# Kernel optimization log

Hardware: AMD Instinct MI355X
Metric: run time of the kernel (lower is better)

The kernel has to match this reference:

```python
import jax, jax.numpy as jnp
import numpy as np

N_FFT = 1024
HOP = 256
WIN = 1024
SIG_LEN = 16777216  # 2**24 samples


def _hamming_sym(M):
    # scipy.signal.hamming(M, sym=True): 0.54 - 0.46*cos(2*pi*n/(M-1))
    n = np.arange(M)
    return (0.54 - 0.46 * np.cos(2.0 * np.pi * n / (M - 1))).astype(np.float32)


def setup_inputs() -> dict:
    key = jax.random.key(0)
    x = jax.random.normal(key, (SIG_LEN,), dtype=jnp.float32)
    return {"x": x}


def reference(x):
    # window, normalized by sqrt(n_fft) (sum of Hamming window is nonzero)
    win = jnp.asarray(_hamming_sym(WIN) / np.sqrt(N_FFT).astype(np.float32))
    hw2 = WIN // 2
    half_n = N_FFT // 2 + 1
    pad = 3 * HOP

    xp = jnp.pad(x, (pad, pad))       # np.append zeros on both sides
    total = xp.shape[0]
    n_rows = total // HOP             # allocated output rows (trailing rows stay zero)
    n_frames = (total - WIN) // HOP + 1  # frames actually computed by the while-loop

    starts = jnp.arange(n_frames) * HOP
    frames = xp[starts[:, None] + jnp.arange(WIN)[None, :]] * win

    # zero-phase buffer: buf[:hw1] = win_x[hw2:], buf[-hw2:] = win_x[:hw2]
    mid = jnp.zeros((n_frames, N_FFT - WIN), dtype=frames.dtype)
    buf = jnp.concatenate([frames[:, hw2:], mid, frames[:, :hw2]], axis=1)

    spec = jnp.fft.rfft(buf, n=N_FFT, axis=1)        # [n_frames, half_n] complex64
    mag = jnp.abs(spec).astype(jnp.float32)
    ph = jnp.angle(spec).astype(jnp.float32)

    xm_x = jnp.zeros((n_rows, half_n), jnp.float32).at[:n_frames].set(mag)
    xp_x = jnp.zeros((n_rows, half_n), jnp.float32).at[:n_frames].set(ph)
    return (xm_x, xp_x)
```

## Files before the change

kernel.cpp:

```cpp
#include <hip/hip_runtime.h>


#define SIG_LEN   16777216
#define N_FRAMES  65539
#define N_ROWS    65542
#define HALF_N    513
#define FRAMES_FLOATS (N_FRAMES * HALF_N)
#define MAG_SZ        (N_ROWS   * HALF_N)


__global__ void init_tables(double* __restrict__ ws) {
  int i = blockIdx.x * 256 + threadIdx.x;
  const double PI = 3.14159265358979323846;
  if (i < 1024) {
    ws[i] = (0.54 - 0.46 * cos(2.0 * PI * (double)i / 1023.0)) / 32.0;
  }
  if (i < 448) {
    int l = i / 7, r = i % 7 + 1;
    double a = -2.0 * PI * (double)(l * r) / 512.0;
    ws[1024 + 2 * i]     = cos(a);
    ws[1024 + 2 * i + 1] = sin(a);
  }
  if (i < 56) {
    int q = i / 7, r = i % 7 + 1;
    double a = -2.0 * PI * (double)(8 * q * r) / 512.0;
    ws[1920 + 2 * i]     = cos(a);
    ws[1920 + 2 * i + 1] = sin(a);
  }
  if (i < 513) {
    double th = PI * (double)i / 512.0;
    double c = cos(th), s = sin(th);
    ws[2048 + 4 * i]     = 0.5 * (1.0 - s);
    ws[2048 + 4 * i + 1] = -0.5 * c;
    ws[2048 + 4 * i + 2] = 0.5 * (1.0 + s);
    ws[2048 + 4 * i + 3] = 0.5 * c;
  }
}

__global__ void zero_tail(float* __restrict__ out) {
  int i = blockIdx.x * 256 + threadIdx.x;
  if (i < (MAG_SZ - FRAMES_FLOATS)) {
    out[FRAMES_FLOATS + i] = 0.0f;
    out[MAG_SZ + FRAMES_FLOATS + i] = 0.0f;
  }
}

#define CMUL(vr, vi, wx, wy) { double _t = (vr)*(wx) - (vi)*(wy); \
                               (vi) = (vr)*(wy) + (vi)*(wx); (vr) = _t; }

__device__ __forceinline__ void dft8(double* ar, double* ai) {
  const double S = 0.70710678118654752440;
  double s0r = ar[0] + ar[4], s0i = ai[0] + ai[4];
  double s1r = ar[0] - ar[4], s1i = ai[0] - ai[4];
  double s2r = ar[2] + ar[6], s2i = ai[2] + ai[6];
  double s3r = ar[2] - ar[6], s3i = ai[2] - ai[6];
  double t0r = ar[1] + ar[5], t0i = ai[1] + ai[5];
  double t1r = ar[1] - ar[5], t1i = ai[1] - ai[5];
  double t2r = ar[3] + ar[7], t2i = ai[3] + ai[7];
  double t3r = ar[3] - ar[7], t3i = ai[3] - ai[7];

  double e0r = s0r + s2r, e0i = s0i + s2i;
  double e2r = s0r - s2r, e2i = s0i - s2i;
  double e1r = s1r + s3i, e1i = s1i - s3r;
  double e3r = s1r - s3i, e3i = s1i + s3r;
  double o0r = t0r + t2r, o0i = t0i + t2i;
  double o2r = t0r - t2r, o2i = t0i - t2i;
  double o1r = t1r + t3i, o1i = t1i - t3r;
  double o3r = t1r - t3i, o3i = t1i + t3r;

  double u1r = S * (o1r + o1i), u1i = S * (o1i - o1r);
  double u2r = o2i,             u2i = -o2r;
  double u3r = S * (o3i - o3r), u3i = -S * (o3r + o3i);

  ar[0] = e0r + o0r; ai[0] = e0i + o0i;
  ar[4] = e0r - o0r; ai[4] = e0i - o0i;
  ar[1] = e1r + u1r; ai[1] = e1i + u1i;
  ar[5] = e1r - u1r; ai[5] = e1i - u1i;
  ar[2] = e2r + u2r; ai[2] = e2i + u2i;
  ar[6] = e2r - u2r; ai[6] = e2i - u2i;
  ar[3] = e3r + u3r; ai[3] = e3i + u3i;
  ar[7] = e3r - u3r; ai[7] = e3i - u3i;
}

__device__ __forceinline__ float fast_atan2f(float y, float x) {
  const float PI   = 3.14159265358979f;
  const float PI_2 = 1.57079632679490f;
  float ax = fabsf(x), ay = fabsf(y);
  float mx = fmaxf(ax, ay), mn = fminf(ax, ay);
  float t = mn * __builtin_amdgcn_rcpf(mx);
  t = (mx == 0.0f) ? 0.0f : t;
  float zz = t * t;
  float a = fmaf(zz, -0.01172120f, 0.05265332f);
  a = fmaf(zz, a, -0.11643287f);
  a = fmaf(zz, a,  0.19354346f);
  a = fmaf(zz, a, -0.33262347f);
  a = fmaf(zz, a,  0.99997726f);
  a = a * t;
  a = (ay > ax) ? (PI_2 - a) : a;
  a = (x < 0.0f) ? (PI - a) : a;
  return copysignf(a, y);
}

__global__ __launch_bounds__(128, 5) void stft_frame(const float* __restrict__ x,
                                                     const double* __restrict__ ws,
                                                     float* __restrict__ out) {
  __shared__ double2 zbuf[2][512];

  const int wv = threadIdx.x >> 6;
  const int l  = threadIdx.x & 63;
  const int f  = blockIdx.x * 2 + wv;
  if (f >= N_FRAMES) return;
  double2* z = zbuf[wv];

  const int g = l >> 3;
  const int q = l & 7;

  double ar[8], ai[8];
  const int base = f * 256 - 768;
  if (base >= 0 && base + 1024 <= SIG_LEN) {
#pragma unroll
    for (int n2 = 0; n2 < 8; ++n2) {
      int j = 128 * n2 + 2 * l;
      float2 xv = *(const float2*)(x + base + j);
      double2 wn = *(const double2*)(ws + j);
      ar[n2] = (double)xv.x * wn.x;
      ai[n2] = (double)xv.y * wn.y;
    }
  } else {
#pragma unroll
    for (int n2 = 0; n2 < 8; ++n2) {
      int j  = 128 * n2 + 2 * l;
      int ix = base + j;
      double v0 = (ix >= 0 && ix < SIG_LEN) ? (double)x[ix] : 0.0;
      double v1 = (ix + 1 >= 0 && ix + 1 < SIG_LEN) ? (double)x[ix + 1] : 0.0;
      double2 wn = *(const double2*)(ws + j);
      ar[n2] = v0 * wn.x;
      ai[n2] = v1 * wn.y;
    }
  }

  dft8(ar, ai);
  {
    const double2* tw1 = (const double2*)(ws + 1024) + l * 7;
#pragma unroll
    for (int r = 1; r < 8; ++r) {
      double2 w = tw1[r - 1];
      CMUL(ar[r], ai[r], w.x, w.y);
    }
  }

#pragma unroll
  for (int r = 0; r < 8; ++r) {
    z[64 * r + 8 * g + (q ^ g)] = make_double2(ar[r], ai[r]);
  }
  asm volatile("s_waitcnt lgkmcnt(0)" ::: "memory");
#pragma unroll
  for (int r = 0; r < 8; ++r) {
    double2 v = z[64 * g + 8 * r + (q ^ r)];
    ar[r] = v.x; ai[r] = v.y;
  }

  dft8(ar, ai);
  {
    const double2* tw2 = (const double2*)(ws + 1920) + q * 7;
#pragma unroll
    for (int r = 1; r < 8; ++r) {
      double2 w = tw2[r - 1];
      CMUL(ar[r], ai[r], w.x, w.y);
    }
  }

#pragma unroll
  for (int r = 0; r < 8; ++r) {
    z[64 * g + 8 * r + (q ^ r)] = make_double2(ar[r], ai[r]);
  }
  asm volatile("s_waitcnt lgkmcnt(0)" ::: "memory");
#pragma unroll
  for (int r = 0; r < 8; ++r) {
    double2 v = z[64 * g + 8 * q + (r ^ q)];
    ar[r] = v.x; ai[r] = v.y;
  }

  dft8(ar, ai);

#pragma unroll
  for (int r = 0; r < 8; ++r) {
    z[64 * r + 8 * q + (g ^ q)] = make_double2(ar[r], ai[r]);
  }
  asm volatile("s_waitcnt lgkmcnt(0)" ::: "memory");

  const double* AB = ws + 2048;
  const int czk = 8 * g + (q ^ g);
  const float sgn = (l & 1) ? -1.0f : 1.0f;
  float* outm = out + f * HALF_N;
  float* outp = out + MAG_SZ + f * HALF_N;
#pragma unroll
  for (int i = 0; i < 4; ++i) {
    int k  = 64 * i + l;
    int km = 512 - k;
    double2 Zk = z[64 * i + czk];
    int zmi = km & 511;
    zmi = (zmi & ~7) | ((zmi ^ (zmi >> 3)) & 7);
    double2 Zm = z[zmi];
    const double* ab = AB + 4 * k;
    double Axv = ab[0], Ayv = ab[1], Bxv = ab[2], Byv = ab[3];
    double Yr  = Zk.x * Axv - Zk.y * Ayv + Zm.x * Bxv + Zm.y * Byv;
    double Yi  = Zk.x * Ayv + Zk.y * Axv + Zm.x * Byv - Zm.y * Bxv;
    double Y2r = Zm.x * Axv + Zm.y * Ayv + Zk.x * Bxv - Zk.y * Byv;
    double Y2i = -(Zm.x * Ayv - Zm.y * Axv + Zk.x * Byv + Zk.y * Bxv);
    if (i == 0) {
      if (l == 0) { Yi = 0.0; Y2i = 0.0; }
    }
    float yr  = (float)Yr,  yi  = (float)Yi;
    float y2r = (float)Y2r, y2i = (float)Y2i;
    float mag1 = __builtin_amdgcn_sqrtf(fmaf(yr, yr, yi * yi));
    float ph1  = fast_atan2f(sgn * yi, sgn * yr);
    float mag2 = __builtin_amdgcn_sqrtf(fmaf(y2r, y2r, y2i * y2i));
    float ph2  = fast_atan2f(sgn * y2i, sgn * y2r);
    outm[k]  = mag1;
    outp[k]  = ph1;
    outm[km] = mag2;
    outp[km] = ph2;
  }

  if (l == 0) {
    double2 zc = z[256];
    float yr = (float)zc.x, yi = (float)(-zc.y);
    outm[256] = __builtin_amdgcn_sqrtf(fmaf(yr, yr, yi * yi));
    outp[256] = fast_atan2f(yi, yr);
  }
}

extern "C" void kernel_launch(void* const* d_in, const int* in_sizes, int n_in,
                              void* d_out, int out_size, void* d_ws, size_t ws_size,
                              hipStream_t stream) {
  const float* x = (const float*)d_in[0];
  float* out = (float*)d_out;
  double* ws = (double*)d_ws;

  hipLaunchKernelGGL(init_tables, dim3(4), dim3(256), 0, stream, ws);
  hipLaunchKernelGGL(zero_tail, dim3(7), dim3(256), 0, stream, out);
  hipLaunchKernelGGL(stft_frame, dim3((N_FRAMES + 1) / 2), dim3(128), 0, stream,
                     x, ws, out);
}
```

Measured before the change: 400.1 us.

## Process two adjacent frames per wavefront, sharing input loads and twiddles

Each 64-thread block now computes two consecutive frames in one wavefront. It loads 10 float2 vectors covering both overlapping windows, so the shared samples are fetched once, and window/twiddle/AB coefficients are applied to both frames. The final-stage output mapping is changed so each lane keeps its own Zk in registers and only the mirrored Zm is read from LDS, with the odd-k sign folded into the AB table. This doubles register pressure per thread (launch bounds 64,4), which may reduce occupancy.

```diff
diff --git a/kernel.cpp b/kernel.cpp
--- a/kernel.cpp
+++ b/kernel.cpp
@@ -30,10 +30,11 @@
   if (i < 513) {
     double th = PI * (double)i / 512.0;
     double c = cos(th), s = sin(th);
-    ws[2048 + 4 * i]     = 0.5 * (1.0 - s);
-    ws[2048 + 4 * i + 1] = -0.5 * c;
-    ws[2048 + 4 * i + 2] = 0.5 * (1.0 + s);
-    ws[2048 + 4 * i + 3] = 0.5 * c;
+    double sg = (i & 1) ? -1.0 : 1.0;
+    ws[2048 + 4 * i]     = sg * 0.5 * (1.0 - s);
+    ws[2048 + 4 * i + 1] = sg * -0.5 * c;
+    ws[2048 + 4 * i + 2] = sg * 0.5 * (1.0 + s);
+    ws[2048 + 4 * i + 3] = sg * 0.5 * c;
   }
 }
 
@@ -101,133 +102,167 @@
   return copysignf(a, y);
 }
 
-__global__ __launch_bounds__(128, 5) void stft_frame(const float* __restrict__ x,
-                                                     const double* __restrict__ ws,
-                                                     float* __restrict__ out) {
-  __shared__ double2 zbuf[2][512];
-
-  const int wv = threadIdx.x >> 6;
-  const int l  = threadIdx.x & 63;
-  const int f  = blockIdx.x * 2 + wv;
-  if (f >= N_FRAMES) return;
-  double2* z = zbuf[wv];
-
+__global__ __launch_bounds__(64, 4) void stft_frame(const float* __restrict__ x,
+                                                    const double* __restrict__ ws,
+                                                    float* __restrict__ out) {
+  __shared__ double2 zA[512];
+  __shared__ double2 zB[512];
+
+  const int l = threadIdx.x;
   const int g = l >> 3;
   const int q = l & 7;
 
-  double ar[8], ai[8];
-  const int base = f * 256 - 768;
-  if (base >= 0 && base + 1024 <= SIG_LEN) {
-#pragma unroll
-    for (int n2 = 0; n2 < 8; ++n2) {
-      int j = 128 * n2 + 2 * l;
-      float2 xv = *(const float2*)(x + base + j);
-      double2 wn = *(const double2*)(ws + j);
-      ar[n2] = (double)xv.x * wn.x;
-      ai[n2] = (double)xv.y * wn.y;
-    }
+  const int fa = blockIdx.x * 2;
+  const int fb = fa + 1;
+  const bool bvalid = (fb < N_FRAMES);
+
+  float2 xv[10];
+  const int baseA = fa * 256 - 768;
+  if (baseA >= 0 && baseA + 1280 <= SIG_LEN) {
+#pragma unroll
+    for (int m = 0; m < 10; ++m)
+      xv[m] = *(const float2*)(x + baseA + 128 * m + 2 * l);
   } else {
 #pragma unroll
-    for (int n2 = 0; n2 < 8; ++n2) {
-      int j  = 128 * n2 + 2 * l;
-      int ix = base + j;
-      double v0 = (ix >= 0 && ix < SIG_LEN) ? (double)x[ix] : 0.0;
-      double v1 = (ix + 1 >= 0 && ix + 1 < SIG_LEN) ? (double)x[ix + 1] : 0.0;
-      double2 wn = *(const double2*)(ws + j);
-      ar[n2] = v0 * wn.x;
-      ai[n2] = v1 * wn.y;
-    }
-  }
-
-  dft8(ar, ai);
+    for (int m = 0; m < 10; ++m) {
+      int ix = baseA + 128 * m + 2 * l;
+      float a0 = (ix >= 0 && ix < SIG_LEN) ? x[ix] : 0.0f;
+      float a1 = (ix + 1 >= 0 && ix + 1 < SIG_LEN) ? x[ix + 1] : 0.0f;
+      xv[m] = make_float2(a0, a1);
+    }
+  }
+
+  double aar[8], aai[8], bar[8], bai[8];
+#pragma unroll
+  for (int n2 = 0; n2 < 8; ++n2) {
+    double2 wn = *(const double2*)(ws + 128 * n2 + 2 * l);
+    aar[n2] = (double)xv[n2].x     * wn.x;
+    aai[n2] = (double)xv[n2].y     * wn.y;
+    bar[n2] = (double)xv[n2 + 2].x * wn.x;
+    bai[n2] = (double)xv[n2 + 2].y * wn.y;
+  }
+
+  dft8(aar, aai);
+  dft8(bar, bai);
   {
     const double2* tw1 = (const double2*)(ws + 1024) + l * 7;
 #pragma unroll
     for (int r = 1; r < 8; ++r) {
       double2 w = tw1[r - 1];
-      CMUL(ar[r], ai[r], w.x, w.y);
-    }
-  }
-
-#pragma unroll
-  for (int r = 0; r < 8; ++r) {
-    z[64 * r + 8 * g + (q ^ g)] = make_double2(ar[r], ai[r]);
+      CMUL(aar[r], aai[r], w.x, w.y);
+      CMUL(bar[r], bai[r], w.x, w.y);
+    }
+  }
+
+#pragma unroll
+  for (int r = 0; r < 8; ++r) {
+    int e = 64 * r + 8 * g + (q ^ g);
+    zA[e] = make_double2(aar[r], aai[r]);
+    zB[e] = make_double2(bar[r], bai[r]);
   }
   asm volatile("s_waitcnt lgkmcnt(0)" ::: "memory");
 #pragma unroll
   for (int r = 0; r < 8; ++r) {
-    double2 v = z[64 * g + 8 * r + (q ^ r)];
-    ar[r] = v.x; ai[r] = v.y;
-  }
-
-  dft8(ar, ai);
+    int e = 64 * g + 8 * r + (q ^ r);
+    double2 va = zA[e], vb = zB[e];
+    aar[r] = va.x; aai[r] = va.y;
+    bar[r] = vb.x; bai[r] = vb.y;
+  }
+
+  dft8(aar, aai);
+  dft8(bar, bai);
   {
     const double2* tw2 = (const double2*)(ws + 1920) + q * 7;
 #pragma unroll
     for (int r = 1; r < 8; ++r) {
       double2 w = tw2[r - 1];
-      CMUL(ar[r], ai[r], w.x, w.y);
-    }
-  }
-
-#pragma unroll
-  for (int r = 0; r < 8; ++r) {
-    z[64 * g + 8 * r + (q ^ r)] = make_double2(ar[r], ai[r]);
+      CMUL(aar[r], aai[r], w.x, w.y);
+      CMUL(bar[r], bai[r], w.x, w.y);
+    }
+  }
+
+#pragma unroll
+  for (int r = 0; r < 8; ++r) {
+    int e = 64 * g + 8 * r + (q ^ r);
+    zA[e] = make_double2(aar[r], aai[r]);
+    zB[e] = make_double2(bar[r], bai[r]);
   }
   asm volatile("s_waitcnt lgkmcnt(0)" ::: "memory");
 #pragma unroll
   for (int r = 0; r < 8; ++r) {
-    double2 v = z[64 * g + 8 * q + (r ^ q)];
-    ar[r] = v.x; ai[r] = v.y;
-  }
-
-  dft8(ar, ai);
-
-#pragma unroll
-  for (int r = 0; r < 8; ++r) {
-    z[64 * r + 8 * q + (g ^ q)] = make_double2(ar[r], ai[r]);
+    int e = 64 * g + 8 * q + (r ^ q);
+    double2 va = zA[e], vb = zB[e];
+    aar[r] = va.x; aai[r] = va.y;
+    bar[r] = vb.x; bai[r] = vb.y;
+  }
+
+  dft8(aar, aai);
+  dft8(bar, bai);
+
+#pragma unroll
+  for (int r = 4; r < 8; ++r) {
+    int e = 64 * (r - 4) + 8 * q + (g ^ q);
+    zA[e] = make_double2(aar[r], aai[r]);
+    zB[e] = make_double2(bar[r], bai[r]);
   }
   asm volatile("s_waitcnt lgkmcnt(0)" ::: "memory");
 
   const double* AB = ws + 2048;
-  const int czk = 8 * g + (q ^ g);
-  const float sgn = (l & 1) ? -1.0f : 1.0f;
-  float* outm = out + f * HALF_N;
-  float* outp = out + MAG_SZ + f * HALF_N;
+  float* outmA = out + fa * HALF_N;
+  float* outpA = out + MAG_SZ + fa * HALF_N;
+  float* outmB = outmA + HALF_N;
+  float* outpB = outpA + HALF_N;
 #pragma unroll
   for (int i = 0; i < 4; ++i) {
-    int k  = 64 * i + l;
+    int k  = 64 * i + 8 * q + g;
     int km = 512 - k;
-    double2 Zk = z[64 * i + czk];
-    int zmi = km & 511;
-    zmi = (zmi & ~7) | ((zmi ^ (zmi >> 3)) & 7);
-    double2 Zm = z[zmi];
+    int addr = ((km - 256) & ~7) | ((km ^ (km >> 3)) & 7);
+    double2 ZmA = zA[addr], ZmB = zB[addr];
+    if (i == 0 && l == 0) {
+      ZmA = make_double2(aar[0], aai[0]);
+      ZmB = make_double2(bar[0], bai[0]);
+    }
     const double* ab = AB + 4 * k;
-    double Axv = ab[0], Ayv = ab[1], Bxv = ab[2], Byv = ab[3];
-    double Yr  = Zk.x * Axv - Zk.y * Ayv + Zm.x * Bxv + Zm.y * Byv;
-    double Yi  = Zk.x * Ayv + Zk.y * Axv + Zm.x * Byv - Zm.y * Bxv;
-    double Y2r = Zm.x * Axv + Zm.y * Ayv + Zk.x * Bxv - Zk.y * Byv;
-    double Y2i = -(Zm.x * Ayv - Zm.y * Axv + Zk.x * Byv + Zk.y * Bxv);
-    if (i == 0) {
-      if (l == 0) { Yi = 0.0; Y2i = 0.0; }
+    double Ax = ab[0], Ay = ab[1], Bx = ab[2], By = ab[3];
+
+    double Yr  = aar[i] * Ax - aai[i] * Ay + ZmA.x * Bx + ZmA.y * By;
+    double Yi  = aar[i] * Ay + aai[i] * Ax + ZmA.x * By - ZmA.y * Bx;
+    double Y2r = ZmA.x * Ax + ZmA.y * Ay + aar[i] * Bx - aai[i] * By;
+    double Y2i = -(ZmA.x * Ay - ZmA.y * Ax + aar[i] * By + aai[i] * Bx);
+
+    double Wr  = bar[i] * Ax - bai[i] * Ay + ZmB.x * Bx + ZmB.y * By;
+    double Wi  = bar[i] * Ay + bai[i] * Ax + ZmB.x * By - ZmB.y * Bx;
+    double W2r = ZmB.x * Ax + ZmB.y * Ay + bar[i] * Bx - bai[i] * By;
+    double W2i = -(ZmB.x * Ay - ZmB.y * Ax + bar[i] * By + bai[i] * Bx);
+
+    if (i == 0 && l == 0) {
+      Yi = 0.0; Y2i = 0.0; Wi = 0.0; W2i = 0.0;
     }
     float yr  = (float)Yr,  yi  = (float)Yi;
     float y2r = (float)Y2r, y2i = (float)Y2i;
-    float mag1 = __builtin_amdgcn_sqrtf(fmaf(yr, yr, yi * yi));
-    float ph1  = fast_atan2f(sgn * yi, sgn * yr);
-    float mag2 = __builtin_amdgcn_sqrtf(fmaf(y2r, y2r, y2i * y2i));
-    float ph2  = fast_atan2f(sgn * y2i, sgn * y2r);
-    outm[k]  = mag1;
-    outp[k]  = ph1;
-    outm[km] = mag2;
-    outp[km] = ph2;
+    outmA[k]  = __builtin_amdgcn_sqrtf(fmaf(yr, yr, yi * yi));
+    outpA[k]  = fast_atan2f(yi, yr);
+    outmA[km] = __builtin_amdgcn_sqrtf(fmaf(y2r, y2r, y2i * y2i));
+    outpA[km] = fast_atan2f(y2i, y2r);
+    if (bvalid) {
+      float wr  = (float)Wr,  wi  = (float)Wi;
+      float w2r = (float)W2r, w2i = (float)W2i;
+      outmB[k]  = __builtin_amdgcn_sqrtf(fmaf(wr, wr, wi * wi));
+      outpB[k]  = fast_atan2f(wi, wr);
+      outmB[km] = __builtin_amdgcn_sqrtf(fmaf(w2r, w2r, w2i * w2i));
+      outpB[km] = fast_atan2f(w2i, w2r);
+    }
   }
 
   if (l == 0) {
-    double2 zc = z[256];
-    float yr = (float)zc.x, yi = (float)(-zc.y);
-    outm[256] = __builtin_amdgcn_sqrtf(fmaf(yr, yr, yi * yi));
-    outp[256] = fast_atan2f(yi, yr);
+    float yr = (float)aar[4], yi = (float)(-aai[4]);
+    outmA[256] = __builtin_amdgcn_sqrtf(fmaf(yr, yr, yi * yi));
+    outpA[256] = fast_atan2f(yi, yr);
+    if (bvalid) {
+      float wr = (float)bar[4], wi = (float)(-bai[4]);
+      outmB[256] = __builtin_amdgcn_sqrtf(fmaf(wr, wr, wi * wi));
+      outpB[256] = fast_atan2f(wi, wr);
+    }
   }
 }
 
@@ -240,6 +275,6 @@
 
   hipLaunchKernelGGL(init_tables, dim3(4), dim3(256), 0, stream, ws);
   hipLaunchKernelGGL(zero_tail, dim3(7), dim3(256), 0, stream, out);
-  hipLaunchKernelGGL(stft_frame, dim3((N_FRAMES + 1) / 2), dim3(128), 0, stream,
+  hipLaunchKernelGGL(stft_frame, dim3((N_FRAMES + 1) / 2), dim3(64), 0, stream,
                      x, ws, out);
 }
```

Measured after the change: 403.2 us. About the same (+0.8%).
